# Performance work log

Measured on AMD Instinct MI355X. Metric: run time of the kernel, lower is better.

The kernel has to match this reference:

```python
import jax, jax.numpy as jnp
import numpy as np

H = 2048  # hidden_size
I = 2048  # input_size
B = 2048  # batch


def setup_inputs() -> dict:
    key = jax.random.key(0)
    k0, k1, k2, k3, k4, k5 = jax.random.split(key, 6)
    # bipolar-domain activations live in [-1, 1]
    inp = jax.random.uniform(k0, (B, I), jnp.float32, minval=-1.0, maxval=1.0)
    hx = jax.random.uniform(k1, (B, H), jnp.float32, minval=-1.0, maxval=1.0)
    s = 1.0 / np.sqrt(H + I)
    w_f = jax.random.normal(k2, (H, H + I), jnp.float32) * s
    b_f = jax.random.normal(k3, (H,), jnp.float32) * s
    w_n = jax.random.normal(k4, (H, H + I), jnp.float32) * s
    b_n = jax.random.normal(k5, (H,), jnp.float32) * s
    return {"input": inp, "hx": hx, "w_f": w_f, "b_f": b_f, "w_n": w_n, "b_n": b_n}


def reference(input, hx, w_f, b_f, w_n, b_n):
    # Expected-value (probability-domain) math of the unary bitstream MGU cell.
    # fg_ug_tanh: FSULinear on [hx, x]; 'hardtanh is direct pass' -> identity act.
    fg_ug_in = jnp.concatenate([hx, input], axis=1)            # [B, H+I]
    fg_in = fg_ug_in @ w_f.T + b_f                              # [B, H]
    # fg_sigmoid: FSUAdd of [fg_in, ones] with scale=None -> (x + 1) / 2
    fg = (fg_in + 1.0) * 0.5                                    # [B, H]
    # fg_hx_mul: FSUMul with static in_1_prob = hx buffer
    fg_hx = fg * hx                                             # [B, H]
    # ng_ug_tanh: FSULinear on [fg*hx, x]
    ng_ug_in = jnp.concatenate([fg_hx, input], axis=1)          # [B, H+I]
    ng = ng_ug_in @ w_n.T + b_n                                 # [B, H]
    # fg_ng_mul: dynamic FSUMul; bipolar bit-inversion (1 - bitstream) negates value
    fg_ng = fg * ng
    # hy_add: FSUAdd([ng, -fg*ng, fg*hx], scale=1) -> plain sum
    hy = ng - fg_ng + fg_hx                                     # = (1-fg)*ng + fg*hx
    return hy
```

## Files before the change

### kernel.cpp

```cpp
#include <hip/hip_runtime.h>
#include <stdint.h>


#define Hdim 2048
#define Idim 2048
#define Bdim 2048
#define Ktot 4096
#define KHALF 2048
#define NSTEP 64
#define NSTEP2 32

typedef __bf16 bf16;
typedef __bf16 bf16x8 __attribute__((ext_vector_type(8)));
typedef float  f32x4  __attribute__((ext_vector_type(4)));

__device__ __forceinline__ void gload_lds16(const bf16* g, bf16* l) {
  __builtin_amdgcn_global_load_lds(
      (const __attribute__((address_space(1))) unsigned int*)g,
      (__attribute__((address_space(3))) unsigned int*)l,
      16, 0, 0);
}

__device__ __forceinline__ void cvt8(const float* __restrict__ src, bf16* __restrict__ dst) {
  const float4* s = (const float4*)src;
  float4 a = s[0], b = s[1];
  bf16x8 o;
  o[0]=(bf16)a.x; o[1]=(bf16)a.y; o[2]=(bf16)a.z; o[3]=(bf16)a.w;
  o[4]=(bf16)b.x; o[5]=(bf16)b.y; o[6]=(bf16)b.z; o[7]=(bf16)b.w;
  *(bf16x8*)dst = o;
}

__global__ void prep_kernel(const float* __restrict__ w_f, const float* __restrict__ w_n,
                            const float* __restrict__ hx, const float* __restrict__ x,
                            bf16* __restrict__ Wf, bf16* __restrict__ Wn,
                            bf16* __restrict__ A1) {
  const int n8 = Hdim * Ktot / 8;
  int stride = gridDim.x * blockDim.x;
  for (int i = blockIdx.x * blockDim.x + threadIdx.x; i < 3 * n8; i += stride) {
    if (i < n8) {
      cvt8(w_f + (size_t)i * 8, Wf + (size_t)i * 8);
    } else if (i < 2 * n8) {
      int j = i - n8;
      cvt8(w_n + (size_t)j * 8, Wn + (size_t)j * 8);
    } else {
      int j = i - 2 * n8;
      int e = j * 8;
      int b = e >> 12;
      int k = e & (Ktot - 1);
      const float* src = (k < Hdim) ? (hx + (size_t)b * Hdim + k)
                                    : (x  + (size_t)b * Idim + (k - Hdim));
      cvt8(src, A1 + (size_t)e);
    }
  }
}

template<int EPI>
__global__ __launch_bounds__(256, 2)
void gemm_kernel(const bf16* __restrict__ Ab0, int sA0,
                 const bf16* __restrict__ Ab1, int sA1,
                 const bf16* __restrict__ W,
                 const float* __restrict__ bias,
                 const float* __restrict__ hx,
                 bf16* __restrict__ OMF,
                 bf16* __restrict__ A2L,
                 float* __restrict__ OUT)
{
  __shared__ bf16 lds[2][12288];

  int bid  = blockIdx.x;
  int sbid = (bid & 7) * 64 + (bid >> 3);
  int tm = sbid >> 5, tn = sbid & 31;

  int tid = threadIdx.x;
  int w = tid >> 6, lane = tid & 63;
  int wrow = (w >> 1) * 64;
  int wcol = (w & 1) * 32;
  int fr = lane & 15, fq = lane >> 4;
  int swz = fr & 7;

  int srow = tid >> 3;
  int csrc = (tid & 7) ^ (srow & 7);

  const bf16* pA0 = Ab0 + (size_t)(tm * 128 + srow) * sA0 + csrc * 8;
  const bf16* pA1 = Ab1 + (size_t)(tm * 128 + srow) * sA1 + csrc * 8;
  const bf16* pB  = W   + (size_t)(tn * 64  + srow) * Ktot + csrc * 8;
  int lb = w * 512;

#define STAGE(buf, t_) do {                                                    \
    const bf16* pa_ = ((t_) < NSTEP2) ? pA0 : pA1;                             \
    size_t sa_ = ((t_) < NSTEP2) ? (size_t)sA0 : (size_t)sA1;                  \
    size_t ko_ = ((t_) < NSTEP2) ? (size_t)(t_) * 64 : (size_t)((t_) - NSTEP2) * 64; \
    _Pragma("unroll")                                                          \
    for (int jj = 0; jj < 4; ++jj)                                             \
      gload_lds16(pa_ + (size_t)jj * 32 * sa_ + ko_, &lds[buf][jj * 2048 + lb]); \
    _Pragma("unroll")                                                          \
    for (int jj = 0; jj < 2; ++jj)                                             \
      gload_lds16(pB + (size_t)jj * 32 * Ktot + (size_t)(t_) * 64,             \
                  &lds[buf][8192 + jj * 2048 + lb]);                           \
  } while (0)

  f32x4 acc[4][2] = {};

  auto compute = [&](int buf) {
    #pragma unroll
    for (int kk = 0; kk < 2; ++kk) {
      bf16x8 af[4], bv[2];
      int ch = ((kk * 4 + fq) ^ swz) * 8;
      #pragma unroll
      for (int m = 0; m < 4; ++m)
        af[m] = *(const bf16x8*)&lds[buf][(wrow + m * 16 + fr) * 64 + ch];
      #pragma unroll
      for (int n = 0; n < 2; ++n)
        bv[n] = *(const bf16x8*)&lds[buf][8192 + (wcol + n * 16 + fr) * 64 + ch];
      __builtin_amdgcn_s_setprio(1);
      #pragma unroll
      for (int m = 0; m < 4; ++m)
        #pragma unroll
        for (int n = 0; n < 2; ++n)
          acc[m][n] = __builtin_amdgcn_mfma_f32_16x16x32_bf16(af[m], bv[n], acc[m][n], 0, 0, 0);
      __builtin_amdgcn_s_setprio(0);
    }
  };

  STAGE(0, 0);
  int cur = 0;
  for (int t = 0; t < NSTEP - 1; ++t) {
    STAGE(cur ^ 1, t + 1);
    asm volatile("s_waitcnt vmcnt(6)" ::: "memory");
    __builtin_amdgcn_s_barrier();
    compute(cur);
    __builtin_amdgcn_s_barrier();
    cur ^= 1;
  }
  asm volatile("s_waitcnt vmcnt(0)" ::: "memory");
  __builtin_amdgcn_s_barrier();
  compute(cur);
#undef STAGE

  int row0 = tm * 128 + wrow + fq * 4;
  int col0 = tn * 64 + wcol + fr;
  #pragma unroll
  for (int n = 0; n < 2; ++n) {
    int gcol = col0 + n * 16;
    float bv2 = bias[gcol];
    #pragma unroll
    for (int m = 0; m < 4; ++m) {
      #pragma unroll
      for (int i = 0; i < 4; ++i) {
        int grow = row0 + m * 16 + i;
        size_t idx = (size_t)grow * Hdim + gcol;
        float v = acc[m][n][i] + bv2;
        if (EPI == 0) {
          float fg = (v + 1.0f) * 0.5f;
          OMF[idx] = (bf16)(1.0f - fg);
          A2L[idx] = (bf16)(fg * hx[idx]);
        } else {
          OUT[idx] = (float)OMF[idx] * v + (float)A2L[idx];
        }
      }
    }
  }
}

extern "C" void kernel_launch(void* const* d_in, const int* in_sizes, int n_in,
                              void* d_out, int out_size, void* d_ws, size_t ws_size,
                              hipStream_t stream) {
  const float* x   = (const float*)d_in[0];
  const float* hx  = (const float*)d_in[1];
  const float* w_f = (const float*)d_in[2];
  const float* b_f = (const float*)d_in[3];
  const float* w_n = (const float*)d_in[4];
  const float* b_n = (const float*)d_in[5];
  float* out = (float*)d_out;

  bf16* A1  = (bf16*)d_ws;
  bf16* A2L = A1  + (size_t)Bdim * Ktot;
  bf16* Wf  = A2L + (size_t)Bdim * KHALF;
  bf16* Wn  = Wf  + (size_t)Hdim * Ktot;
  bf16* OMF = Wn  + (size_t)Hdim * Ktot;

  prep_kernel<<<2048, 256, 0, stream>>>(w_f, w_n, hx, x, Wf, Wn, A1);

  gemm_kernel<0><<<512, 256, 0, stream>>>(A1, Ktot, A1 + KHALF, Ktot, Wf, b_f,
                                          hx, OMF, A2L, nullptr);
  gemm_kernel<1><<<512, 256, 0, stream>>>(A2L, KHALF, A1 + Hdim, Ktot, Wn, b_n,
                                          nullptr, OMF, A2L, out);
}
```

Baseline: 112.9 us.

## Pre-pack weights in MFMA fragment order and load B directly to registers

The prep kernel now writes the bf16 weights in a fragment-packed layout matching the 16x16x32 MFMA B operand. The GEMM loads B fragments straight from global memory into registers, double-buffered across iterations, and no longer stages them through LDS. This shrinks LDS use and removes the B LDS reads and writes. The trade-off is that waves sharing a column tile duplicate their global B loads, and the extra loads in flight add register pressure.

```diff
diff --git a/kernel.cpp b/kernel.cpp
--- a/kernel.cpp
+++ b/kernel.cpp
@@ -32,16 +32,21 @@
 
 __global__ void prep_kernel(const float* __restrict__ w_f, const float* __restrict__ w_n,
                             const float* __restrict__ hx, const float* __restrict__ x,
-                            bf16* __restrict__ Wf, bf16* __restrict__ Wn,
+                            bf16* __restrict__ Wfp, bf16* __restrict__ Wnp,
                             bf16* __restrict__ A1) {
   const int n8 = Hdim * Ktot / 8;
   int stride = gridDim.x * blockDim.x;
   for (int i = blockIdx.x * blockDim.x + threadIdx.x; i < 3 * n8; i += stride) {
-    if (i < n8) {
-      cvt8(w_f + (size_t)i * 8, Wf + (size_t)i * 8);
-    } else if (i < 2 * n8) {
-      int j = i - n8;
-      cvt8(w_n + (size_t)j * 8, Wn + (size_t)j * 8);
+    if (i < 2 * n8) {
+      int j = (i < n8) ? i : i - n8;
+      const float* wsrc = (i < n8) ? w_f : w_n;
+      bf16* wdst = (i < n8) ? Wfp : Wnp;
+      int c  = j >> 13;
+      int rem = j & 8191;
+      int kb = rem >> 6;
+      int l  = rem & 63;
+      const float* src = wsrc + ((size_t)c * 16 + (l & 15)) * Ktot + kb * 32 + (l >> 4) * 8;
+      cvt8(src, wdst + (size_t)j * 8);
     } else {
       int j = i - 2 * n8;
       int e = j * 8;
@@ -58,14 +63,14 @@
 __global__ __launch_bounds__(256, 2)
 void gemm_kernel(const bf16* __restrict__ Ab0, int sA0,
                  const bf16* __restrict__ Ab1, int sA1,
-                 const bf16* __restrict__ W,
+                 const bf16* __restrict__ Wp,
                  const float* __restrict__ bias,
                  const float* __restrict__ hx,
                  bf16* __restrict__ OMF,
                  bf16* __restrict__ A2L,
                  float* __restrict__ OUT)
 {
-  __shared__ bf16 lds[2][12288];
+  __shared__ bf16 lds[2][8192];
 
   int bid  = blockIdx.x;
   int sbid = (bid & 7) * 64 + (bid >> 3);
@@ -80,62 +85,74 @@
 
   int srow = tid >> 3;
   int csrc = (tid & 7) ^ (srow & 7);
-
   const bf16* pA0 = Ab0 + (size_t)(tm * 128 + srow) * sA0 + csrc * 8;
   const bf16* pA1 = Ab1 + (size_t)(tm * 128 + srow) * sA1 + csrc * 8;
-  const bf16* pB  = W   + (size_t)(tn * 64  + srow) * Ktot + csrc * 8;
   int lb = w * 512;
 
-#define STAGE(buf, t_) do {                                                    \
+  const bf16* pW = Wp + ((size_t)(tn * 4 + (wcol >> 4))) * 65536 + lane * 8;
+
+#define STAGE_A(buf, t_) do {                                                  \
     const bf16* pa_ = ((t_) < NSTEP2) ? pA0 : pA1;                             \
     size_t sa_ = ((t_) < NSTEP2) ? (size_t)sA0 : (size_t)sA1;                  \
     size_t ko_ = ((t_) < NSTEP2) ? (size_t)(t_) * 64 : (size_t)((t_) - NSTEP2) * 64; \
     _Pragma("unroll")                                                          \
     for (int jj = 0; jj < 4; ++jj)                                             \
       gload_lds16(pa_ + (size_t)jj * 32 * sa_ + ko_, &lds[buf][jj * 2048 + lb]); \
+  } while (0)
+
+#define BLOAD(dst, t_) do {                                                    \
+    size_t o_ = (size_t)(t_) * 1024;                                           \
+    dst[0] = *(const bf16x8*)(pW + o_);                                        \
+    dst[1] = *(const bf16x8*)(pW + o_ + 65536);                                \
+    dst[2] = *(const bf16x8*)(pW + o_ + 512);                                  \
+    dst[3] = *(const bf16x8*)(pW + o_ + 512 + 65536);                          \
+  } while (0)
+
+  f32x4 acc[4][2] = {};
+
+#define COMPUTE(buf, B_) do {                                                  \
     _Pragma("unroll")                                                          \
-    for (int jj = 0; jj < 2; ++jj)                                             \
-      gload_lds16(pB + (size_t)jj * 32 * Ktot + (size_t)(t_) * 64,             \
-                  &lds[buf][8192 + jj * 2048 + lb]);                           \
-  } while (0)
-
-  f32x4 acc[4][2] = {};
-
-  auto compute = [&](int buf) {
-    #pragma unroll
-    for (int kk = 0; kk < 2; ++kk) {
-      bf16x8 af[4], bv[2];
-      int ch = ((kk * 4 + fq) ^ swz) * 8;
-      #pragma unroll
-      for (int m = 0; m < 4; ++m)
-        af[m] = *(const bf16x8*)&lds[buf][(wrow + m * 16 + fr) * 64 + ch];
-      #pragma unroll
-      for (int n = 0; n < 2; ++n)
-        bv[n] = *(const bf16x8*)&lds[buf][8192 + (wcol + n * 16 + fr) * 64 + ch];
-      __builtin_amdgcn_s_setprio(1);
-      #pragma unroll
-      for (int m = 0; m < 4; ++m)
-        #pragma unroll
-        for (int n = 0; n < 2; ++n)
-          acc[m][n] = __builtin_amdgcn_mfma_f32_16x16x32_bf16(af[m], bv[n], acc[m][n], 0, 0, 0);
-      __builtin_amdgcn_s_setprio(0);
-    }
-  };
-
-  STAGE(0, 0);
-  int cur = 0;
-  for (int t = 0; t < NSTEP - 1; ++t) {
-    STAGE(cur ^ 1, t + 1);
-    asm volatile("s_waitcnt vmcnt(6)" ::: "memory");
-    __builtin_amdgcn_s_barrier();
-    compute(cur);
-    __builtin_amdgcn_s_barrier();
-    cur ^= 1;
+    for (int kk = 0; kk < 2; ++kk) {                                           \
+      bf16x8 af[4];                                                            \
+      int ch = ((kk * 4 + fq) ^ swz) * 8;                                      \
+      _Pragma("unroll")                                                        \
+      for (int m = 0; m < 4; ++m)                                              \
+        af[m] = *(const bf16x8*)&lds[buf][(wrow + m * 16 + fr) * 64 + ch];     \
+      __builtin_amdgcn_s_setprio(1);                                           \
+      _Pragma("unroll")                                                        \
+      for (int m = 0; m < 4; ++m)                                              \
+        _Pragma("unroll")                                                      \
+        for (int n = 0; n < 2; ++n)                                            \
+          acc[m][n] = __builtin_amdgcn_mfma_f32_16x16x32_bf16(af[m], B_[kk * 2 + n], acc[m][n], 0, 0, 0); \
+      __builtin_amdgcn_s_setprio(0);                                           \
+    }                                                                          \
+  } while (0)
+
+#define ITER(t_, buf, bcur, bnext) do {                                        \
+    if ((t_) + 1 < NSTEP) {                                                    \
+      STAGE_A((buf) ^ 1, (t_) + 1);                                            \
+      BLOAD(bnext, (t_) + 1);                                                  \
+      asm volatile("s_waitcnt vmcnt(8)" ::: "memory");   \
+    } else {                                                                   \
+      asm volatile("s_waitcnt vmcnt(0)" ::: "memory");                         \
+    }                                                                          \
+    __builtin_amdgcn_s_barrier();                                              \
+    COMPUTE(buf, bcur);                                                        \
+    __builtin_amdgcn_s_barrier();                                              \
+  } while (0)
+
+  bf16x8 bA[4], bB[4];
+  BLOAD(bA, 0);
+  STAGE_A(0, 0);
+  #pragma unroll 1
+  for (int th = 0; th < NSTEP / 2; ++th) {
+    ITER(2 * th,     0, bA, bB);
+    ITER(2 * th + 1, 1, bB, bA);
   }
-  asm volatile("s_waitcnt vmcnt(0)" ::: "memory");
-  __builtin_amdgcn_s_barrier();
-  compute(cur);
-#undef STAGE
+#undef ITER
+#undef COMPUTE
+#undef BLOAD
+#undef STAGE_A
 
   int row0 = tm * 128 + wrow + fq * 4;
   int col0 = tn * 64 + wcol + fr;
@@ -175,14 +192,14 @@
 
   bf16* A1  = (bf16*)d_ws;
   bf16* A2L = A1  + (size_t)Bdim * Ktot;
-  bf16* Wf  = A2L + (size_t)Bdim * KHALF;
-  bf16* Wn  = Wf  + (size_t)Hdim * Ktot;
-  bf16* OMF = Wn  + (size_t)Hdim * Ktot;
-
-  prep_kernel<<<2048, 256, 0, stream>>>(w_f, w_n, hx, x, Wf, Wn, A1);
-
-  gemm_kernel<0><<<512, 256, 0, stream>>>(A1, Ktot, A1 + KHALF, Ktot, Wf, b_f,
+  bf16* Wfp = A2L + (size_t)Bdim * KHALF;
+  bf16* Wnp = Wfp + (size_t)Hdim * Ktot;
+  bf16* OMF = Wnp + (size_t)Hdim * Ktot;
+
+  prep_kernel<<<2048, 256, 0, stream>>>(w_f, w_n, hx, x, Wfp, Wnp, A1);
+
+  gemm_kernel<0><<<512, 256, 0, stream>>>(A1, Ktot, A1 + KHALF, Ktot, Wfp, b_f,
                                           hx, OMF, A2L, nullptr);
-  gemm_kernel<1><<<512, 256, 0, stream>>>(A2L, KHALF, A1 + Hdim, Ktot, Wn, b_n,
+  gemm_kernel<1><<<512, 256, 0, stream>>>(A2L, KHALF, A1 + Hdim, Ktot, Wnp, b_n,
                                           nullptr, OMF, A2L, out);
 }
```

New measurement: 123.8 us. 9.7% more time.

## Split-K GEMM with 128x128 tiles, ticket-based reduction, and fused Wn conversion

Applied to the files above, without the earlier changes.

Each GEMM now uses 128x128 output tiles with two blocks per tile, each covering one half of K. Both write fp32 partials, and the second block to finish (found through an atomic ticket) adds the other block's partial and runs the epilogue. The first finisher of the first GEMM converts a slice of w_n to bf16, which moves that work out of the prep kernel and overlaps it with the GEMM. The goal is more data reuse per block and better overlap. The cost is extra fp32 partial traffic, atomics and fences, and a launch-bounds change that may lower occupancy.

```diff
diff --git a/kernel.cpp b/kernel.cpp
--- a/kernel.cpp
+++ b/kernel.cpp
@@ -7,8 +7,7 @@
 #define Bdim 2048
 #define Ktot 4096
 #define KHALF 2048
-#define NSTEP 64
-#define NSTEP2 32
+#define NSTEP (KHALF / 64)
 
 typedef __bf16 bf16;
 typedef __bf16 bf16x8 __attribute__((ext_vector_type(8)));
@@ -30,20 +29,21 @@
   *(bf16x8*)dst = o;
 }
 
-__global__ void prep_kernel(const float* __restrict__ w_f, const float* __restrict__ w_n,
+__global__ void prep_kernel(const float* __restrict__ w_f,
                             const float* __restrict__ hx, const float* __restrict__ x,
-                            bf16* __restrict__ Wf, bf16* __restrict__ Wn,
-                            bf16* __restrict__ A1) {
+                            bf16* __restrict__ Wf, bf16* __restrict__ A1,
+                            int* __restrict__ tickets) {
+  if (blockIdx.x == 0) {
+    tickets[threadIdx.x] = 0;
+    tickets[threadIdx.x + 256] = 0;
+  }
   const int n8 = Hdim * Ktot / 8;
   int stride = gridDim.x * blockDim.x;
-  for (int i = blockIdx.x * blockDim.x + threadIdx.x; i < 3 * n8; i += stride) {
+  for (int i = blockIdx.x * blockDim.x + threadIdx.x; i < 2 * n8; i += stride) {
     if (i < n8) {
       cvt8(w_f + (size_t)i * 8, Wf + (size_t)i * 8);
-    } else if (i < 2 * n8) {
+    } else {
       int j = i - n8;
-      cvt8(w_n + (size_t)j * 8, Wn + (size_t)j * 8);
-    } else {
-      int j = i - 2 * n8;
       int e = j * 8;
       int b = e >> 12;
       int k = e & (Ktot - 1);
@@ -55,68 +55,72 @@
 }
 
 template<int EPI>
-__global__ __launch_bounds__(256, 2)
+__global__ __launch_bounds__(256)
 void gemm_kernel(const bf16* __restrict__ Ab0, int sA0,
                  const bf16* __restrict__ Ab1, int sA1,
                  const bf16* __restrict__ W,
                  const float* __restrict__ bias,
                  const float* __restrict__ hx,
+                 const float* __restrict__ wn_src,
+                 bf16* __restrict__ wn_dst,
                  bf16* __restrict__ OMF,
                  bf16* __restrict__ A2L,
-                 float* __restrict__ OUT)
+                 float* P0, float* P1,
+                 int* __restrict__ ticket,
+                 float* OUT)
 {
-  __shared__ bf16 lds[2][12288];
-
-  int bid  = blockIdx.x;
-  int sbid = (bid & 7) * 64 + (bid >> 3);
-  int tm = sbid >> 5, tn = sbid & 31;
-
-  int tid = threadIdx.x;
-  int w = tid >> 6, lane = tid & 63;
-  int wrow = (w >> 1) * 64;
-  int wcol = (w & 1) * 32;
+  __shared__ bf16 lds[2][2][8192];
+  __shared__ int s_old;
+
+  int bid   = blockIdx.x;
+  int tile  = bid >> 1;
+  int kpart = bid & 1;
+  int sbid = (tile & 7) * 32 + (tile >> 3);
+  int tm = sbid >> 4, tn = sbid & 15;
+
+  int tid  = threadIdx.x;
+  int sub = tid >> 6, lane = tid & 63;
+  int wrow = (sub >> 1) * 64;
+  int wcol = (sub & 1) * 64;
   int fr = lane & 15, fq = lane >> 4;
   int swz = fr & 7;
 
   int srow = tid >> 3;
   int csrc = (tid & 7) ^ (srow & 7);
 
-  const bf16* pA0 = Ab0 + (size_t)(tm * 128 + srow) * sA0 + csrc * 8;
-  const bf16* pA1 = Ab1 + (size_t)(tm * 128 + srow) * sA1 + csrc * 8;
-  const bf16* pB  = W   + (size_t)(tn * 64  + srow) * Ktot + csrc * 8;
-  int lb = w * 512;
-
-#define STAGE(buf, t_) do {                                                    \
-    const bf16* pa_ = ((t_) < NSTEP2) ? pA0 : pA1;                             \
-    size_t sa_ = ((t_) < NSTEP2) ? (size_t)sA0 : (size_t)sA1;                  \
-    size_t ko_ = ((t_) < NSTEP2) ? (size_t)(t_) * 64 : (size_t)((t_) - NSTEP2) * 64; \
+  const bf16* pA = (kpart == 0)
+      ? Ab0 + (size_t)(tm * 128 + srow) * sA0 + csrc * 8
+      : Ab1 + (size_t)(tm * 128 + srow) * sA1 + csrc * 8;
+  const size_t strA = (kpart == 0) ? (size_t)sA0 : (size_t)sA1;
+  const bf16* pB = W + (size_t)(tn * 128 + srow) * Ktot + csrc * 8 + kpart * KHALF;
+  int lbase = sub * 512;
+
+#define STAGE(buf, koff) do {                                                  \
     _Pragma("unroll")                                                          \
-    for (int jj = 0; jj < 4; ++jj)                                             \
-      gload_lds16(pa_ + (size_t)jj * 32 * sa_ + ko_, &lds[buf][jj * 2048 + lb]); \
-    _Pragma("unroll")                                                          \
-    for (int jj = 0; jj < 2; ++jj)                                             \
-      gload_lds16(pB + (size_t)jj * 32 * Ktot + (size_t)(t_) * 64,             \
-                  &lds[buf][8192 + jj * 2048 + lb]);                           \
+    for (int jj = 0; jj < 4; ++jj) {                                           \
+      gload_lds16(pA + (size_t)jj * 32 * strA + (koff), &lds[buf][0][jj * 2048 + lbase]); \
+      gload_lds16(pB + (size_t)jj * 32 * Ktot + (koff), &lds[buf][1][jj * 2048 + lbase]); \
+    }                                                                          \
   } while (0)
 
-  f32x4 acc[4][2] = {};
+  f32x4 acc[4][4] = {};
 
   auto compute = [&](int buf) {
     #pragma unroll
     for (int kk = 0; kk < 2; ++kk) {
-      bf16x8 af[4], bv[2];
+      bf16x8 af[4], bv[4];
       int ch = ((kk * 4 + fq) ^ swz) * 8;
       #pragma unroll
       for (int m = 0; m < 4; ++m)
-        af[m] = *(const bf16x8*)&lds[buf][(wrow + m * 16 + fr) * 64 + ch];
-      #pragma unroll
-      for (int n = 0; n < 2; ++n)
-        bv[n] = *(const bf16x8*)&lds[buf][8192 + (wcol + n * 16 + fr) * 64 + ch];
+        af[m] = *(const bf16x8*)&lds[buf][0][(wrow + m * 16 + fr) * 64 + ch];
+      #pragma unroll
+      for (int n = 0; n < 4; ++n)
+        bv[n] = *(const bf16x8*)&lds[buf][1][(wcol + n * 16 + fr) * 64 + ch];
       __builtin_amdgcn_s_setprio(1);
       #pragma unroll
       for (int m = 0; m < 4; ++m)
         #pragma unroll
-        for (int n = 0; n < 2; ++n)
+        for (int n = 0; n < 4; ++n)
           acc[m][n] = __builtin_amdgcn_mfma_f32_16x16x32_bf16(af[m], bv[n], acc[m][n], 0, 0, 0);
       __builtin_amdgcn_s_setprio(0);
     }
@@ -125,8 +129,8 @@
   STAGE(0, 0);
   int cur = 0;
   for (int t = 0; t < NSTEP - 1; ++t) {
-    STAGE(cur ^ 1, t + 1);
-    asm volatile("s_waitcnt vmcnt(6)" ::: "memory");
+    STAGE(cur ^ 1, (t + 1) * 64);
+    asm volatile("s_waitcnt vmcnt(8)" ::: "memory");
     __builtin_amdgcn_s_barrier();
     compute(cur);
     __builtin_amdgcn_s_barrier();
@@ -137,10 +141,35 @@
   compute(cur);
 #undef STAGE
 
+  float* Pme = kpart ? P1 : P0;
   int row0 = tm * 128 + wrow + fq * 4;
-  int col0 = tn * 64 + wcol + fr;
+  int col0 = tn * 128 + wcol + fr;
   #pragma unroll
-  for (int n = 0; n < 2; ++n) {
+  for (int n = 0; n < 4; ++n)
+    #pragma unroll
+    for (int m = 0; m < 4; ++m)
+      #pragma unroll
+      for (int i = 0; i < 4; ++i)
+        Pme[(size_t)(row0 + m * 16 + i) * Hdim + col0 + n * 16] = acc[m][n][i];
+
+  __threadfence();
+  __syncthreads();
+  if (tid == 0) s_old = atomicAdd(ticket + tile, 1);
+  __syncthreads();
+  if (s_old == 0) {
+    if (EPI == 0) {
+      const int CH = (Hdim * Ktot / 8) / 256;
+      size_t base = (size_t)tile * CH;
+      for (int c = tid; c < CH; c += 256)
+        cvt8(wn_src + (base + c) * 8, wn_dst + (base + c) * 8);
+    }
+    return;
+  }
+  __threadfence();
+
+  const float* Po = kpart ? P0 : P1;
+  #pragma unroll
+  for (int n = 0; n < 4; ++n) {
     int gcol = col0 + n * 16;
     float bv2 = bias[gcol];
     #pragma unroll
@@ -149,7 +178,7 @@
       for (int i = 0; i < 4; ++i) {
         int grow = row0 + m * 16 + i;
         size_t idx = (size_t)grow * Hdim + gcol;
-        float v = acc[m][n][i] + bv2;
+        float v = acc[m][n][i] + Po[idx] + bv2;
         if (EPI == 0) {
           float fg = (v + 1.0f) * 0.5f;
           OMF[idx] = (bf16)(1.0f - fg);
@@ -178,11 +207,16 @@
   bf16* Wf  = A2L + (size_t)Bdim * KHALF;
   bf16* Wn  = Wf  + (size_t)Hdim * Ktot;
   bf16* OMF = Wn  + (size_t)Hdim * Ktot;
-
-  prep_kernel<<<2048, 256, 0, stream>>>(w_f, w_n, hx, x, Wf, Wn, A1);
+  float* P1 = (float*)(OMF + (size_t)Bdim * Hdim);
+  int* tickets = (int*)(P1 + (size_t)Bdim * Hdim);
+  float* P0 = out;
+
+  prep_kernel<<<2048, 256, 0, stream>>>(w_f, hx, x, Wf, A1, tickets);
 
   gemm_kernel<0><<<512, 256, 0, stream>>>(A1, Ktot, A1 + KHALF, Ktot, Wf, b_f,
-                                          hx, OMF, A2L, nullptr);
+                                          hx, w_n, Wn, OMF, A2L,
+                                          P0, P1, tickets, nullptr);
   gemm_kernel<1><<<512, 256, 0, stream>>>(A2L, KHALF, A1 + Hdim, Ktot, Wn, b_n,
-                                          nullptr, OMF, A2L, out);
-}
+                                          nullptr, nullptr, nullptr, OMF, A2L,
+                                          P0, P1, tickets + 256, out);
+}
```

New measurement: 411.8 us. +264.6%, slower.

## Triple-buffer LDS tiles with prefetch distance two and one barrier per step

Applied to the files above, without the earlier changes.

Replaces the double-buffered K loop with a three-buffer ring in LDS. Loads for step t+2 are issued right after the barrier, and the trailing barrier is dropped, so each iteration needs one barrier instead of two and global loads get more time in flight. LDS per block rises from 48KB to 72KB, which may limit the two-blocks-per-CU occupancy target. The vmcnt accounting also has to stay correct across the rotating buffers.

```diff
diff --git a/kernel.cpp b/kernel.cpp
--- a/kernel.cpp
+++ b/kernel.cpp
@@ -65,7 +65,7 @@
                  bf16* __restrict__ A2L,
                  float* __restrict__ OUT)
 {
-  __shared__ bf16 lds[2][12288];
+  __shared__ bf16 lds[3][12288];
 
   int bid  = blockIdx.x;
   int sbid = (bid & 7) * 64 + (bid >> 3);
@@ -86,55 +86,59 @@
   const bf16* pB  = W   + (size_t)(tn * 64  + srow) * Ktot + csrc * 8;
   int lb = w * 512;
 
-#define STAGE(buf, t_) do {                                                    \
+#define STAGE(pbuf, t_) do {                                                   \
     const bf16* pa_ = ((t_) < NSTEP2) ? pA0 : pA1;                             \
     size_t sa_ = ((t_) < NSTEP2) ? (size_t)sA0 : (size_t)sA1;                  \
     size_t ko_ = ((t_) < NSTEP2) ? (size_t)(t_) * 64 : (size_t)((t_) - NSTEP2) * 64; \
     _Pragma("unroll")                                                          \
     for (int jj = 0; jj < 4; ++jj)                                             \
-      gload_lds16(pa_ + (size_t)jj * 32 * sa_ + ko_, &lds[buf][jj * 2048 + lb]); \
+      gload_lds16(pa_ + (size_t)jj * 32 * sa_ + ko_, (pbuf) + jj * 2048 + lb); \
     _Pragma("unroll")                                                          \
     for (int jj = 0; jj < 2; ++jj)                                             \
       gload_lds16(pB + (size_t)jj * 32 * Ktot + (size_t)(t_) * 64,             \
-                  &lds[buf][8192 + jj * 2048 + lb]);                           \
+                  (pbuf) + 8192 + jj * 2048 + lb);                             \
   } while (0)
 
   f32x4 acc[4][2] = {};
 
-  auto compute = [&](int buf) {
-    #pragma unroll
-    for (int kk = 0; kk < 2; ++kk) {
-      bf16x8 af[4], bv[2];
-      int ch = ((kk * 4 + fq) ^ swz) * 8;
-      #pragma unroll
-      for (int m = 0; m < 4; ++m)
-        af[m] = *(const bf16x8*)&lds[buf][(wrow + m * 16 + fr) * 64 + ch];
-      #pragma unroll
-      for (int n = 0; n < 2; ++n)
-        bv[n] = *(const bf16x8*)&lds[buf][8192 + (wcol + n * 16 + fr) * 64 + ch];
-      __builtin_amdgcn_s_setprio(1);
-      #pragma unroll
-      for (int m = 0; m < 4; ++m)
-        #pragma unroll
-        for (int n = 0; n < 2; ++n)
-          acc[m][n] = __builtin_amdgcn_mfma_f32_16x16x32_bf16(af[m], bv[n], acc[m][n], 0, 0, 0);
-      __builtin_amdgcn_s_setprio(0);
-    }
-  };
+#define COMPUTE(pbuf) do {                                                     \
+    _Pragma("unroll")                                                          \
+    for (int kk = 0; kk < 2; ++kk) {                                           \
+      bf16x8 af[4], bv[2];                                                     \
+      int ch = ((kk * 4 + fq) ^ swz) * 8;                                      \
+      _Pragma("unroll")                                                        \
+      for (int m = 0; m < 4; ++m)                                              \
+        af[m] = *(const bf16x8*)((pbuf) + (wrow + m * 16 + fr) * 64 + ch);     \
+      _Pragma("unroll")                                                        \
+      for (int n = 0; n < 2; ++n)                                              \
+        bv[n] = *(const bf16x8*)((pbuf) + 8192 + (wcol + n * 16 + fr) * 64 + ch); \
+      __builtin_amdgcn_s_setprio(1);                                           \
+      _Pragma("unroll")                                                        \
+      for (int m = 0; m < 4; ++m)                                              \
+        _Pragma("unroll")                                                      \
+        for (int n = 0; n < 2; ++n)                                            \
+          acc[m][n] = __builtin_amdgcn_mfma_f32_16x16x32_bf16(af[m], bv[n], acc[m][n], 0, 0, 0); \
+      __builtin_amdgcn_s_setprio(0);                                           \
+    }                                                                          \
+  } while (0)
 
-  STAGE(0, 0);
-  int cur = 0;
-  for (int t = 0; t < NSTEP - 1; ++t) {
-    STAGE(cur ^ 1, t + 1);
-    asm volatile("s_waitcnt vmcnt(6)" ::: "memory");
+  bf16* p0 = &lds[0][0];
+  bf16* p1 = &lds[1][0];
+  bf16* p2 = &lds[2][0];
+
+  STAGE(p0, 0);
+  STAGE(p1, 1);
+  #pragma unroll 1
+  for (int t = 0; t < NSTEP; ++t) {
+    if (t < NSTEP - 1) asm volatile("s_waitcnt vmcnt(6)" ::: "memory");
+    else               asm volatile("s_waitcnt vmcnt(0)" ::: "memory");
     __builtin_amdgcn_s_barrier();
-    compute(cur);
-    __builtin_amdgcn_s_barrier();
-    cur ^= 1;
+    asm volatile("" ::: "memory");
+    if (t + 2 < NSTEP) STAGE(p2, t + 2);
+    COMPUTE(p0);
+    bf16* tmp = p0; p0 = p1; p1 = p2; p2 = tmp;
   }
-  asm volatile("s_waitcnt vmcnt(0)" ::: "memory");
-  __builtin_amdgcn_s_barrier();
-  compute(cur);
+#undef COMPUTE
 #undef STAGE
 
   int row0 = tm * 128 + wrow + fq * 4;
```

Measured after the change: 115.1 us. No clear change (+1.9%).
